# Performance work log

Hardware: AMD Instinct MI355X
Metric: run time of the kernel (lower is better)

## Reference

```python
import jax, jax.numpy as jnp
import numpy as np

MAX_ITER = 3
DAMPING = 1e-3
HUBER_B = 0.02
LAMBDA_ICP, LAMBDA_RGB = 1.0, 1e-6
DIST_THRESH = 0.1


def pixel_grid(H, W):
    j, i = jnp.meshgrid(jnp.arange(H, dtype=jnp.float32), jnp.arange(W, dtype=jnp.float32), indexing='ij')
    return i, j  # i = x (col), j = y (row)


def compute_vertex(depth, K):
    fx, fy, cx, cy = K[0, 0], K[1, 1], K[0, 2], K[1, 2]
    H, W = depth.shape
    i, j = pixel_grid(H, W)
    return jnp.stack([(i - cx) / fx, (j - cy) / fy, jnp.ones_like(i)], -1) * depth[..., None]


def sobel(img, normalize=True):
    # replicate-padded 3x3 Sobel cross-correlation, img [H,W,C]
    p = jnp.pad(img, ((1, 1), (1, 1), (0, 0)), mode='edge')
    dx = (p[:-2, 2:] - p[:-2, :-2]) + 2.0 * (p[1:-1, 2:] - p[1:-1, :-2]) + (p[2:, 2:] - p[2:, :-2])
    dy = (p[2:, :-2] - p[:-2, :-2]) + 2.0 * (p[2:, 1:-1] - p[:-2, 1:-1]) + (p[2:, 2:] - p[:-2, 2:])
    if normalize:
        mag = jnp.sqrt(dx * dx + dy * dy + 1e-8)
        dx, dy = dx / mag, dy / mag
    return dx, dy


def compute_normal(vmap_):
    dx, dy = sobel(vmap_, normalize=False)
    n = jnp.cross(dx, dy)
    n = n / (jnp.linalg.norm(n, axis=-1, keepdims=True) + 1e-8)
    d = vmap_[..., 2]
    invalid = (d <= d.min()) | (d >= d.max())
    return jnp.where(invalid[..., None], 0.0, n)


def warp_jacobian(depth, K):
    fx, fy, cx, cy = K[0, 0], K[1, 1], K[0, 2], K[1, 2]
    H, W = depth.shape
    i, j = pixel_grid(H, W)
    x = (i - cx) / fx * depth
    y = (j - cy) / fy * depth
    invD = 1.0 / depth
    invD2 = invD * invD
    xy = x * y
    O = jnp.zeros_like(depth)
    dx_dp = jnp.stack([-invD2 * xy, 1.0 + x * x * invD2, -y * invD, invD, O, -invD2 * x], -1)
    dy_dp = jnp.stack([-1.0 - invD2 * y * y, xy * invD2, x * invD, O, invD, -invD2 * y], -1)
    return dx_dp * fx, dy_dp * fy


def bilinear(feat, u, v):
    # grid_sample(mode=bilinear, padding=border, align_corners=True) on pixel coords
    H, W, _ = feat.shape
    u = jnp.clip(u, 0.0, W - 1.0)
    v = jnp.clip(v, 0.0, H - 1.0)
    u0 = jnp.floor(u)
    v0 = jnp.floor(v)
    wu = (u - u0)[..., None]
    wv = (v - v0)[..., None]
    u0i = u0.astype(jnp.int32)
    v0i = v0.astype(jnp.int32)
    u1i = jnp.minimum(u0i + 1, W - 1)
    v1i = jnp.minimum(v0i + 1, H - 1)
    f00 = feat[v0i, u0i]
    f01 = feat[v0i, u1i]
    f10 = feat[v1i, u0i]
    f11 = feat[v1i, u1i]
    return (f00 * (1 - wu) + f01 * wu) * (1 - wv) + (f10 * (1 - wu) + f11 * wu) * wv


def project(vt, K, H, W):
    z = vt[..., 2]
    u = vt[..., 0] / z * K[0, 0] + K[0, 2]
    v = vt[..., 1] / z * K[1, 1] + K[1, 2]
    inview = (u > 0) & (u < W - 1) & (v > 0) & (v < H - 1) & (z > 0)
    return u, v, inview


def huber_weight(x, b=HUBER_B):
    rho = jnp.where(x <= b, x * x, 2.0 * b * x - b * b)
    x_safe = jnp.where(x < 1e-8, 1.0, x)
    return jnp.sqrt(rho + 1e-16) / x_safe


def skew(w):
    z = jnp.zeros((), w.dtype)
    return jnp.stack([jnp.stack([z, -w[2], w[1]]), jnp.stack([w[2], z, -w[0]]), jnp.stack([-w[1], w[0], z])])


def exp_so3(w):
    Wh = skew(w)
    th2 = jnp.maximum(jnp.sum(w * w), 1e-30)
    th = jnp.sqrt(th2)
    R = jnp.eye(3, dtype=w.dtype) + Wh * (jnp.sin(th) / th) + (Wh @ Wh) * ((1.0 - jnp.cos(th)) / th2)
    return jnp.where(th <= 1e-10, jnp.eye(3, dtype=w.dtype), R)


def icp_residuals(vertex0, vertex1, normal1, mask0, pose, K):
    H, W, _ = vertex0.shape
    R, t = pose[:3, :3], pose[:3, 3]
    v0t = vertex0 @ R.T + t  # [H,W,3]
    u, v, inview = project(v0t, K, H, W)
    v1w = bilinear(vertex1, u, v)
    n1w = bilinear(normal1, u, v)
    diff = v0t - v1w
    valid = inview & mask0 & (v1w[..., 2] > 0) & (jnp.linalg.norm(diff, axis=-1) < DIST_THRESH)
    res = jnp.where(valid, jnp.sum(n1w * diff, -1), 0.0)  # point-to-plane
    J = jnp.where(valid[..., None], jnp.concatenate([jnp.cross(v0t, n1w), n1w], -1), 0.0)  # [H,W,6]
    w = huber_weight(jnp.abs(res))
    return (w * res).reshape(-1, 1), (w[..., None] * J).reshape(-1, 1, 6)


def rgb_residuals(pose, vertex0, x0, x1, K, mask0):
    H, W, _ = x0.shape
    R, t = pose[:3, :3], pose[:3, 3]
    v0t = vertex0 @ R.T + t
    u, v, inview = project(v0t, K, H, W)
    x1w = bilinear(x1, u, v)
    invalid = (~inview) | (~mask0)
    res = jnp.where(invalid[..., None], 0.0, x1w - x0)
    return res, invalid


def inverse_update_pose(Hm, Rhs, pose):
    xi = (jnp.linalg.inv(Hm) @ Rhs).reshape(-1)
    dR = exp_so3(-xi[:3])
    dt = -dR @ xi[3:]
    R1 = dR @ pose[:3, :3]
    t1 = dR @ pose[:3, 3] + dt
    top = jnp.concatenate([R1, t1[:, None]], 1)
    return jnp.concatenate([top, pose[3:4, :]], 0)


def color_icp(pose10, depth0, depth1, x0, x1, K):
    H, W, C = x0.shape
    vertex0 = compute_vertex(depth0, K)
    normal0 = compute_normal(vertex0)  # computed as in original
    mask0 = depth0 > 0.0
    vertex1 = compute_vertex(depth1, K)
    normal1 = compute_normal(vertex1)
    # pre-computable inverse-compositional RGB jacobian: normalized image grads x warp jacobian
    gx, gy = sobel(x0, normalize=True)  # [H,W,C]
    Jx, Jy = warp_jacobian(depth0, K)  # [H,W,6]
    J_rgb_pre = gx[..., None] * Jx[:, :, None, :] + gy[..., None] * Jy[:, :, None, :]  # [H,W,C,6]
    pose = pose10
    for _ in range(MAX_ITER):
        r_icp, J_icp = icp_residuals(vertex0, vertex1, normal1, mask0, pose, K)
        JtWJ = LAMBDA_ICP * jnp.einsum('nci,ncj->ij', J_icp, J_icp)
        JtR = LAMBDA_ICP * jnp.einsum('nci,nc->i', J_icp, r_icp)
        r_rgb, invalid = rgb_residuals(pose, vertex0, x0, x1, K, mask0)
        J_rgb = jnp.where(invalid[..., None, None], 0.0, J_rgb_pre).reshape(-1, C, 6)
        JtWJ = JtWJ + LAMBDA_RGB * jnp.einsum('nci,ncj->ij', J_rgb, J_rgb)
        JtR = JtR + LAMBDA_RGB * jnp.einsum('nci,nc->i', J_rgb, r_rgb.reshape(-1, C))
        Hm = JtWJ + jnp.eye(6) * (jnp.trace(JtWJ) * DAMPING)  # Levenberg-Marquardt damping
        pose = inverse_update_pose(Hm, JtR.reshape(6, 1), pose)
    return pose


def setup_inputs() -> dict:
    key = jax.random.key(0)
    k = jax.random.split(key, 6)
    H, W = 960, 1280
    depth0 = 0.5 + 2.5 * jax.random.uniform(k[0], (H, W), jnp.float32)
    depth1 = 0.5 + 2.5 * jax.random.uniform(k[1], (H, W), jnp.float32)
    x0 = jax.random.uniform(k[2], (H, W, 3), jnp.float32)
    x1 = jax.random.uniform(k[3], (H, W, 3), jnp.float32)
    K = jnp.array([[1050.0, 0.0, (W - 1) / 2.0], [0.0, 1050.0, (H - 1) / 2.0], [0.0, 0.0, 1.0]], jnp.float32)
    w = 0.01 * jax.random.normal(k[4], (3,), jnp.float32)
    t = 0.01 * jax.random.normal(k[5], (3,), jnp.float32)
    R = exp_so3(w)
    pose10 = jnp.concatenate([jnp.concatenate([R, t[:, None]], 1),
                              jnp.array([[0.0, 0.0, 0.0, 1.0]], jnp.float32)], 0)
    return {'pose10': pose10, 'depth0': depth0, 'depth1': depth1, 'x0': x0, 'x1': x1, 'K': K}


def reference(pose10, depth0, depth1, x0, x1, K):
    return color_icp(pose10, depth0, depth1, x0, x1, K)
```

## Files before the change

kernel.cpp:

```cpp
#include <hip/hip_runtime.h>
#include <math.h>

#define HH 960
#define WW 1280
#define NPIX (HH*WW)
#define BPR (WW/256)
#define NBLK_ROW (NPIX/256)
#define NBLK_MAIN (NPIX/(256*4))
#define TROWS 6
#define TW 258
#define PSTRIDE 28

#define WS_POSE_OFF    0
#define WS_PARTIAL_OFF 128
#define WS_NX_OFF      134528

__device__ __forceinline__ int clampi(int v, int lo, int hi){ return v<lo?lo:(v>hi?hi:v); }

__device__ __forceinline__ float pack2h(float a, float b){
  _Float16 ha = (_Float16)a, hb = (_Float16)b;
  unsigned int u = ((unsigned int)__builtin_bit_cast(unsigned short, hb) << 16)
                 |  (unsigned int)__builtin_bit_cast(unsigned short, ha);
  return __builtin_bit_cast(float, u);
}
__device__ __forceinline__ float2 unpack2h(float p){
  unsigned int u = __builtin_bit_cast(unsigned int, p);
  _Float16 ha = __builtin_bit_cast(_Float16, (unsigned short)(u & 0xffffu));
  _Float16 hb = __builtin_bit_cast(_Float16, (unsigned short)(u >> 16));
  return make_float2((float)ha, (float)hb);
}

__global__ __launch_bounds__(256) void k_pre(const float* __restrict__ depth1,
                                             const float* __restrict__ x1,
                                             const float* __restrict__ Kd,
                                             const float* __restrict__ pose_in,
                                             float* __restrict__ pose,
                                             float* __restrict__ nx1){
  int t = threadIdx.x;
  if (blockIdx.x == 0 && t < 16) pose[t] = pose_in[t];
  int bid = blockIdx.x;
  int py = bid / BPR;
  int px = (bid % BPR)*256 + t;
  float fx = Kd[0], fy = Kd[4], cx = Kd[2], cy = Kd[5];
  float invfx = 1.f/fx, invfy = 1.f/fy;
  float vx[3][3], vy[3][3], vz[3][3];
  #pragma unroll
  for (int dr = 0; dr < 3; dr++){
    int r = clampi(py + dr - 1, 0, HH-1);
    #pragma unroll
    for (int dc = 0; dc < 3; dc++){
      int c = clampi(px + dc - 1, 0, WW-1);
      float d = depth1[r*WW + c];
      vx[dr][dc] = ((float)c - cx)*invfx*d;
      vy[dr][dc] = ((float)r - cy)*invfy*d;
      vz[dr][dc] = d;
    }
  }
  float ax_ = (vx[0][2]-vx[0][0]) + 2.f*(vx[1][2]-vx[1][0]) + (vx[2][2]-vx[2][0]);
  float ay_ = (vy[0][2]-vy[0][0]) + 2.f*(vy[1][2]-vy[1][0]) + (vy[2][2]-vy[2][0]);
  float az_ = (vz[0][2]-vz[0][0]) + 2.f*(vz[1][2]-vz[1][0]) + (vz[2][2]-vz[2][0]);
  float bx_ = (vx[2][0]-vx[0][0]) + 2.f*(vx[2][1]-vx[0][1]) + (vx[2][2]-vx[0][2]);
  float by_ = (vy[2][0]-vy[0][0]) + 2.f*(vy[2][1]-vy[0][1]) + (vy[2][2]-vy[0][2]);
  float bz_ = (vz[2][0]-vz[0][0]) + 2.f*(vz[2][1]-vz[0][1]) + (vz[2][2]-vz[0][2]);
  float nx = ay_*bz_ - az_*by_;
  float ny = az_*bx_ - ax_*bz_;
  float nz = ax_*by_ - ay_*bx_;
  float nrm = sqrtf(nx*nx + ny*ny + nz*nz) + 1e-8f;
  float rn  = __builtin_amdgcn_rcpf(nrm);
  nx *= rn; ny *= rn; nz *= rn;
  float dcen = vz[1][1];
  int idx = py*WW + px;
  const float* q = &x1[idx*3];
  float4 a;
  a.x = dcen;
  a.y = pack2h(nx, ny);
  a.z = pack2h(nz, q[0]);
  a.w = pack2h(q[1], q[2]);
  ((float4*)nx1)[idx] = a;
}

__global__ __launch_bounds__(256) void k_main(const float* __restrict__ depth0,
                                              const float* __restrict__ x0,
                                              const float* __restrict__ nx1,
                                              const float* __restrict__ Kd,
                                              const float* __restrict__ pose,
                                              float* __restrict__ partial){
  int t = threadIdx.x;
  int bid = (blockIdx.x & 7)*(NBLK_MAIN/8) + (blockIdx.x >> 3);
  int pr = bid / BPR;
  int cs = bid % BPR;
  int py0 = pr*4;
  int colbase = cs*256 - 1;
  int px = cs*256 + t;

  __shared__ float tile[TROWS*TW*3];
  for (int s = t; s < TROWS*TW; s += 256){
    int r = s / TW, c = s - r*TW;
    int gr = clampi(py0 - 1 + r, 0, HH-1);
    int gc = clampi(colbase + c, 0, WW-1);
    const float* q = &x0[(gr*WW + gc)*3];
    tile[s*3+0] = q[0]; tile[s*3+1] = q[1]; tile[s*3+2] = q[2];
  }

  int idx0 = py0*WW + px;
  float d0v[4];
  #pragma unroll
  for (int kp = 0; kp < 4; kp++) d0v[kp] = depth0[idx0 + kp*WW];
  __syncthreads();

  float fx = Kd[0], fy = Kd[4], cx = Kd[2], cy = Kd[5];
  float inv_fx = 1.f/fx, inv_fy = 1.f/fy;
  float R00=pose[0], R01=pose[1], R02=pose[2],  tx=pose[3];
  float R10=pose[4], R11=pose[5], R12=pose[6],  ty=pose[7];
  float R20=pose[8], R21=pose[9], R22=pose[10], tz=pose[11];

  float acc[27];
  #pragma unroll
  for (int k = 0; k < 27; k++) acc[k] = 0.f;

  const float4* nx4 = (const float4*)nx1;

  #pragma unroll
  for (int kp = 0; kp < 4; kp++){
    int py = py0 + kp;

    float d0 = d0v[kp];
    bool m0 = d0 > 0.f;
    float v0x = ((float)px - cx)*inv_fx*d0;
    float v0y = ((float)py - cy)*inv_fy*d0;
    float v0z = d0;
    float X = R00*v0x + R01*v0y + R02*v0z + tx;
    float Y = R10*v0x + R11*v0y + R12*v0z + ty;
    float Z = R20*v0x + R21*v0y + R22*v0z + tz;
    float invZ = __builtin_amdgcn_rcpf(Z);
    invZ = invZ*(2.0f - Z*invZ);
    float u = X*invZ*fx + cx;
    float v = Y*invZ*fy + cy;
    bool inview = (u > 0.f) && (u < (float)(WW-1)) && (v > 0.f) && (v < (float)(HH-1)) && (Z > 0.f);

    float uc = fminf(fmaxf(u, 0.f), (float)(WW-1));
    float vc = fminf(fmaxf(v, 0.f), (float)(HH-1));
    float u0f = floorf(uc), v0f = floorf(vc);
    float wu = uc - u0f, wv = vc - v0f;
    int u0i = clampi((int)u0f, 0, WW-1);
    int v0i = clampi((int)v0f, 0, HH-1);
    int u1i = min(u0i + 1, WW-1);
    int v1i = min(v0i + 1, HH-1);
    int i00 = v0i*WW + u0i, i01 = v0i*WW + u1i, i10 = v1i*WW + u0i, i11 = v1i*WW + u1i;
    float w00 = (1.f-wu)*(1.f-wv), w01 = wu*(1.f-wv), w10 = (1.f-wu)*wv, w11 = wu*wv;

    float4 p00 = nx4[i00], p01 = nx4[i01], p10 = nx4[i10], p11v = nx4[i11];

    float2 nab00 = unpack2h(p00.y), nzr00 = unpack2h(p00.z);
    float2 nab01 = unpack2h(p01.y), nzr01 = unpack2h(p01.z);
    float2 nab10 = unpack2h(p10.y), nzr10 = unpack2h(p10.z);
    float2 nab11 = unpack2h(p11v.y), nzr11 = unpack2h(p11v.z);

    float t0 = w00*p00.x, t1 = w01*p01.x, t2 = w10*p10.x, t3 = w11*p11v.x;
    float u0c = ((float)u0i - cx)*inv_fx, u1c = ((float)u1i - cx)*inv_fx;
    float v0c = ((float)v0i - cy)*inv_fy, v1c = ((float)v1i - cy)*inv_fy;
    float s2 = (t0+t1)+(t2+t3);
    float s0 = u0c*(t0+t2) + u1c*(t1+t3);
    float s1 = v0c*(t0+t1) + v1c*(t2+t3);
    float nx = nab00.x*w00 + nab01.x*w01 + nab10.x*w10 + nab11.x*w11;
    float ny = nab00.y*w00 + nab01.y*w01 + nab10.y*w10 + nab11.y*w11;
    float nz = nzr00.x*w00 + nzr01.x*w01 + nzr10.x*w10 + nzr11.x*w11;

    float dfx = X - s0, dfy = Y - s1, dfz = Z - s2;
    bool valid = inview && m0 && (s2 > 0.f) && (dfx*dfx + dfy*dfy + dfz*dfz < 0.01f);
    float res = 0.f;
    float J[6] = {0.f,0.f,0.f,0.f,0.f,0.f};
    if (valid){
      res = nx*dfx + ny*dfy + nz*dfz;
      J[0] = Y*nz - Z*ny;
      J[1] = Z*nx - X*nz;
      J[2] = X*ny - Y*nx;
      J[3] = nx; J[4] = ny; J[5] = nz;
    }
    float axv = fabsf(res);
    float rho = (axv <= 0.02f) ? axv*axv : (0.04f*axv - 0.0004f);
    float xs  = (axv < 1e-8f) ? 1.f : axv;
    float hw  = sqrtf(rho + 1e-16f) * __builtin_amdgcn_rcpf(xs);
    float wr  = hw*res;
    float wJ[6];
    #pragma unroll
    for (int i = 0; i < 6; i++) wJ[i] = hw*J[i];
    {
      int k = 0;
      #pragma unroll
      for (int i = 0; i < 6; i++)
        #pragma unroll
        for (int j = i; j < 6; j++)
          acc[k++] += wJ[i]*wJ[j];
      #pragma unroll
      for (int i = 0; i < 6; i++) acc[21+i] += wJ[i]*wr;
    }

    if (inview && m0){
      float2 gb00 = unpack2h(p00.w), gb01 = unpack2h(p01.w);
      float2 gb10 = unpack2h(p10.w), gb11 = unpack2h(p11v.w);
      float xw[3];
      xw[0] = nzr00.y*w00 + nzr01.y*w01 + nzr10.y*w10 + nzr11.y*w11;
      xw[1] = gb00.x*w00 + gb01.x*w01 + gb10.x*w10 + gb11.x*w11;
      xw[2] = gb00.y*w00 + gb01.y*w01 + gb10.y*w10 + gb11.y*w11;

      float ga = 0.f, gb = 0.f, gc2 = 0.f, rx = 0.f, ry = 0.f;
      #pragma unroll
      for (int ch = 0; ch < 3; ch++){
        float p00l = tile[((kp+0)*TW + (t+0))*3 + ch];
        float p01l = tile[((kp+0)*TW + (t+1))*3 + ch];
        float p02l = tile[((kp+0)*TW + (t+2))*3 + ch];
        float p10l = tile[((kp+1)*TW + (t+0))*3 + ch];
        float p11l = tile[((kp+1)*TW + (t+1))*3 + ch];
        float p12l = tile[((kp+1)*TW + (t+2))*3 + ch];
        float p20l = tile[((kp+2)*TW + (t+0))*3 + ch];
        float p21l = tile[((kp+2)*TW + (t+1))*3 + ch];
        float p22l = tile[((kp+2)*TW + (t+2))*3 + ch];
        float dx = (p02l-p00l) + 2.f*(p12l-p10l) + (p22l-p20l);
        float dy = (p20l-p00l) + 2.f*(p21l-p01l) + (p22l-p02l);
        float rinv = __builtin_amdgcn_rsqf(dx*dx + dy*dy + 1e-8f);
        float gx = dx*rinv, gy = dy*rinv;
        float rr = xw[ch] - p11l;
        ga  += gx*gx; gb += gx*gy; gc2 += gy*gy;
        rx  += gx*rr; ry += gy*rr;
      }
      ga *= 1e-6f; gb *= 1e-6f; gc2 *= 1e-6f; rx *= 1e-6f; ry *= 1e-6f;

      float invD = __builtin_amdgcn_rcpf(d0), invD2 = invD*invD;
      float xy = v0x*v0y;
      float Jx[6] = { fx*(-invD2*xy), fx*(1.f + v0x*v0x*invD2), fx*(-v0y*invD), fx*invD, 0.f, fx*(-invD2*v0x) };
      float Jy[6] = { fy*(-1.f - invD2*v0y*v0y), fy*(xy*invD2), fy*(v0x*invD), 0.f, fy*invD, fy*(-invD2*v0y) };
      float P[6], Q[6];
      #pragma unroll
      for (int i = 0; i < 6; i++){ P[i] = ga*Jx[i] + gb*Jy[i]; Q[i] = gb*Jx[i] + gc2*Jy[i]; }
      int k = 0;
      #pragma unroll
      for (int i = 0; i < 6; i++)
        #pragma unroll
        for (int j = i; j < 6; j++)
          acc[k++] += Jx[j]*P[i] + Jy[j]*Q[i];
      #pragma unroll
      for (int i = 0; i < 6; i++) acc[21+i] += Jx[i]*rx + Jy[i]*ry;
    }
  }

  __shared__ float lds[108];
  int lane = t & 63;
  int wid  = t >> 6;
  #pragma unroll
  for (int k = 0; k < 27; k++){
    float vv = acc[k];
    vv += __shfl_down(vv, 32); vv += __shfl_down(vv, 16); vv += __shfl_down(vv, 8);
    vv += __shfl_down(vv, 4);  vv += __shfl_down(vv, 2);  vv += __shfl_down(vv, 1);
    if (lane == 0) lds[wid*27 + k] = vv;
  }
  __syncthreads();
  if (t < 27)
    partial[bid*PSTRIDE + t] = lds[t] + lds[27+t] + lds[54+t] + lds[81+t];
  else if (t == 27)
    partial[bid*PSTRIDE + 27] = 0.f;
}

__global__ __launch_bounds__(256) void k_solve(const float* __restrict__ partial,
                                               float* __restrict__ pose,
                                               float* __restrict__ outp){
  int t = threadIdx.x;
  double acc[PSTRIDE];
  #pragma unroll
  for (int k = 0; k < PSTRIDE; k++) acc[k] = 0.0;
  const float4* p4 = (const float4*)partial;
  for (int r = t; r < NBLK_MAIN; r += 256){
    #pragma unroll
    for (int q = 0; q < 7; q++){
      float4 vv = p4[r*7 + q];
      acc[q*4+0] += (double)vv.x;
      acc[q*4+1] += (double)vv.y;
      acc[q*4+2] += (double)vv.z;
      acc[q*4+3] += (double)vv.w;
    }
  }
  __shared__ double lds[4*PSTRIDE];
  int lane = t & 63, wid = t >> 6;
  #pragma unroll
  for (int k = 0; k < PSTRIDE; k++){
    double vv = acc[k];
    vv += __shfl_down(vv, 32); vv += __shfl_down(vv, 16); vv += __shfl_down(vv, 8);
    vv += __shfl_down(vv, 4);  vv += __shfl_down(vv, 2);  vv += __shfl_down(vv, 1);
    if (lane == 0) lds[wid*PSTRIDE + k] = vv;
  }
  __syncthreads();
  if (t == 0){
    double s[PSTRIDE];
    #pragma unroll
    for (int k = 0; k < PSTRIDE; k++)
      s[k] = lds[k] + lds[PSTRIDE+k] + lds[2*PSTRIDE+k] + lds[3*PSTRIDE+k];
    double Hm[6][6], b[6];
    {
      int k = 0;
      for (int i = 0; i < 6; i++)
        for (int j = i; j < 6; j++){ Hm[i][j] = s[k]; Hm[j][i] = s[k]; k++; }
      for (int i = 0; i < 6; i++) b[i] = s[21+i];
    }
    double tr = Hm[0][0]+Hm[1][1]+Hm[2][2]+Hm[3][3]+Hm[4][4]+Hm[5][5];
    for (int i = 0; i < 6; i++) Hm[i][i] += tr*0.001;
    double A[6][7];
    for (int i = 0; i < 6; i++){
      for (int j = 0; j < 6; j++) A[i][j] = Hm[i][j];
      A[i][6] = b[i];
    }
    for (int c = 0; c < 6; c++){
      int piv = c; double best = fabs(A[c][c]);
      for (int r = c+1; r < 6; r++){ double a = fabs(A[r][c]); if (a > best){ best = a; piv = r; } }
      if (piv != c)
        for (int j = 0; j < 7; j++){ double tv = A[c][j]; A[c][j] = A[piv][j]; A[piv][j] = tv; }
      double inv = 1.0/A[c][c];
      for (int r = 0; r < 6; r++){
        if (r == c) continue;
        double f = A[r][c]*inv;
        for (int j = c; j < 7; j++) A[r][j] -= f*A[c][j];
      }
    }
    double xi[6];
    for (int i = 0; i < 6; i++) xi[i] = A[i][6]/A[i][i];
    double wx = -xi[0], wy = -xi[1], wz = -xi[2];
    double th2 = wx*wx + wy*wy + wz*wz;
    if (th2 < 1e-30) th2 = 1e-30;
    double th = sqrt(th2);
    double dR[3][3];
    if (th <= 1e-10){
      dR[0][0]=1; dR[0][1]=0; dR[0][2]=0;
      dR[1][0]=0; dR[1][1]=1; dR[1][2]=0;
      dR[2][0]=0; dR[2][1]=0; dR[2][2]=1;
    } else {
      double sa = sin(th)/th;
      double sb = (1.0 - cos(th))/th2;
      double Wm[3][3] = {{0,-wz,wy},{wz,0,-wx},{-wy,wx,0}};
      double W2[3][3];
      for (int i = 0; i < 3; i++)
        for (int j = 0; j < 3; j++)
          W2[i][j] = Wm[i][0]*Wm[0][j] + Wm[i][1]*Wm[1][j] + Wm[i][2]*Wm[2][j];
      for (int i = 0; i < 3; i++)
        for (int j = 0; j < 3; j++)
          dR[i][j] = (i==j ? 1.0 : 0.0) + sa*Wm[i][j] + sb*W2[i][j];
    }
    double dt[3];
    for (int i = 0; i < 3; i++)
      dt[i] = -(dR[i][0]*xi[3] + dR[i][1]*xi[4] + dR[i][2]*xi[5]);
    double Ro[3][3], to[3];
    for (int i = 0; i < 3; i++){
      for (int j = 0; j < 3; j++) Ro[i][j] = (double)pose[i*4+j];
      to[i] = (double)pose[i*4+3];
    }
    double Rn[3][3], tn[3];
    for (int i = 0; i < 3; i++){
      for (int j = 0; j < 3; j++)
        Rn[i][j] = dR[i][0]*Ro[0][j] + dR[i][1]*Ro[1][j] + dR[i][2]*Ro[2][j];
      tn[i] = dR[i][0]*to[0] + dR[i][1]*to[1] + dR[i][2]*to[2] + dt[i];
    }
    float o16[16];
    for (int i = 0; i < 3; i++){
      for (int j = 0; j < 3; j++) o16[i*4+j] = (float)Rn[i][j];
      o16[i*4+3] = (float)tn[i];
    }
    o16[12] = 0.f; o16[13] = 0.f; o16[14] = 0.f; o16[15] = 1.f;
    for (int k = 0; k < 16; k++){ pose[k] = o16[k]; outp[k] = o16[k]; }
  }
}

extern "C" void kernel_launch(void* const* d_in, const int* in_sizes, int n_in,
                              void* d_out, int out_size, void* d_ws, size_t ws_size,
                              hipStream_t stream) {
  const float* pose10 = (const float*)d_in[0];
  const float* depth0 = (const float*)d_in[1];
  const float* depth1 = (const float*)d_in[2];
  const float* x0     = (const float*)d_in[3];
  const float* x1     = (const float*)d_in[4];
  const float* Kd     = (const float*)d_in[5];
  char* ws = (char*)d_ws;
  float* pose    = (float*)(ws + WS_POSE_OFF);
  float* partial = (float*)(ws + WS_PARTIAL_OFF);
  float* nx1     = (float*)(ws + WS_NX_OFF);
  float* outp    = (float*)d_out;

  hipLaunchKernelGGL(k_pre, dim3(NBLK_ROW), dim3(256), 0, stream,
                     depth1, x1, Kd, pose10, pose, nx1);
  for (int it = 0; it < 3; it++){
    hipLaunchKernelGGL(k_main,  dim3(NBLK_MAIN), dim3(256), 0, stream,
                       depth0, x0, nx1, Kd, pose, partial);
    hipLaunchKernelGGL(k_solve, dim3(1),         dim3(256), 0, stream, partial, pose, outp);
  }
}
```

Before: 218.8 us.

## Replace per-iteration solve kernels with atomic sums and redundant in-block pose solve

Each k_main block now atomically adds its 27 reduced sums into a small per-iteration buffer. At the start of each iteration, one wave per block replays the chain of 6x6 solves and pose updates from the original pose, which removes the separate single-block solve launch between iterations. A single final solve kernel writes the output pose. The cost is float atomics, which make summation order nondeterministic, a solve done in float rather than double without pivoting, and redundant solve work in every block.

```diff
diff --git a/kernel.cpp b/kernel.cpp
--- a/kernel.cpp
+++ b/kernel.cpp
@@ -9,11 +9,9 @@
 #define NBLK_MAIN (NPIX/(256*4))
 #define TROWS 6
 #define TW 258
-#define PSTRIDE 28
-
-#define WS_POSE_OFF    0
-#define WS_PARTIAL_OFF 128
-#define WS_NX_OFF      134528
+
+#define WS_S_OFF   0
+#define WS_NX_OFF  512
 
 __device__ __forceinline__ int clampi(int v, int lo, int hi){ return v<lo?lo:(v>hi?hi:v); }
 
@@ -30,14 +28,84 @@
   return make_float2((float)ha, (float)hb);
 }
 
+__device__ __forceinline__ void wave_chain_solve(const float* __restrict__ S, int nsteps,
+                                                 const float* __restrict__ pose_in,
+                                                 float* sp, int lane){
+  if (lane < 12) sp[lane] = pose_in[lane];
+  int r = lane < 6 ? lane : 5;
+  for (int step = 0; step < nsteps; ++step){
+    const float* s = S + step*32;
+    float a[7];
+    #pragma unroll
+    for (int j = 0; j < 6; j++){
+      int i = r < j ? r : j, J = r < j ? j : r;
+      a[j] = s[6*i - (i*(i-1))/2 + (J - i)];
+    }
+    a[6] = s[21 + r];
+    float tr = s[0]+s[6]+s[11]+s[15]+s[18]+s[20];
+    float damp = tr*0.001f;
+    #pragma unroll
+    for (int j = 0; j < 6; j++) a[j] += (r == j) ? damp : 0.f;
+    float mydiag = 1.f;
+    #pragma unroll
+    for (int c = 0; c < 6; c++){
+      float pv[7];
+      #pragma unroll
+      for (int j = 0; j < 7; j++) pv[j] = __shfl(a[j], c);
+      float f = a[c] * (1.0f/pv[c]);
+      bool self = (r == c);
+      if (self) mydiag = a[c];
+      float fr = self ? 0.f : f;
+      #pragma unroll
+      for (int j = 0; j < 7; j++) a[j] -= fr*pv[j];
+    }
+    float xir = a[6] / mydiag;
+    float xi[6];
+    #pragma unroll
+    for (int j = 0; j < 6; j++) xi[j] = __shfl(xir, j);
+    float wx = -xi[0], wy = -xi[1], wz = -xi[2];
+    float th2 = wx*wx + wy*wy + wz*wz; if (th2 < 1e-30f) th2 = 1e-30f;
+    float th = sqrtf(th2);
+    float dR[9];
+    if (th <= 1e-10f){
+      dR[0]=1.f;dR[1]=0.f;dR[2]=0.f; dR[3]=0.f;dR[4]=1.f;dR[5]=0.f; dR[6]=0.f;dR[7]=0.f;dR[8]=1.f;
+    } else {
+      float sa = sinf(th)/th, sb = (1.f - cosf(th))/th2;
+      float cI = 1.f - sb*th2;
+      dR[0]=cI + sb*wx*wx;    dR[1]=sb*wx*wy - sa*wz; dR[2]=sb*wx*wz + sa*wy;
+      dR[3]=sb*wy*wx + sa*wz; dR[4]=cI + sb*wy*wy;    dR[5]=sb*wy*wz - sa*wx;
+      dR[6]=sb*wz*wx - sa*wy; dR[7]=sb*wz*wy + sa*wx; dR[8]=cI + sb*wz*wz;
+    }
+    float dt0 = -(dR[0]*xi[3] + dR[1]*xi[4] + dR[2]*xi[5]);
+    float dt1 = -(dR[3]*xi[3] + dR[4]*xi[4] + dR[5]*xi[5]);
+    float dt2 = -(dR[6]*xi[3] + dR[7]*xi[4] + dR[8]*xi[5]);
+    float Ro[12];
+    #pragma unroll
+    for (int j = 0; j < 12; j++) Ro[j] = sp[j];
+    float Pn[12];
+    #pragma unroll
+    for (int i = 0; i < 3; i++){
+      #pragma unroll
+      for (int j = 0; j < 3; j++)
+        Pn[i*4+j] = dR[i*3+0]*Ro[0*4+j] + dR[i*3+1]*Ro[1*4+j] + dR[i*3+2]*Ro[2*4+j];
+      Pn[i*4+3] = dR[i*3+0]*Ro[3] + dR[i*3+1]*Ro[7] + dR[i*3+2]*Ro[11]
+                + (i==0 ? dt0 : (i==1 ? dt1 : dt2));
+    }
+    if (lane == 0){
+      sp[0]=Pn[0]; sp[1]=Pn[1]; sp[2]=Pn[2];  sp[3]=Pn[3];
+      sp[4]=Pn[4]; sp[5]=Pn[5]; sp[6]=Pn[6];  sp[7]=Pn[7];
+      sp[8]=Pn[8]; sp[9]=Pn[9]; sp[10]=Pn[10]; sp[11]=Pn[11];
+    }
+  }
+}
+
 __global__ __launch_bounds__(256) void k_pre(const float* __restrict__ depth1,
                                              const float* __restrict__ x1,
                                              const float* __restrict__ Kd,
-                                             const float* __restrict__ pose_in,
-                                             float* __restrict__ pose,
+                                             float* __restrict__ S,
                                              float* __restrict__ nx1){
   int t = threadIdx.x;
-  if (blockIdx.x == 0 && t < 16) pose[t] = pose_in[t];
+  if (blockIdx.x == 0 && t < 96) S[t] = 0.f;
   int bid = blockIdx.x;
   int py = bid / BPR;
   int px = (bid % BPR)*256 + t;
@@ -83,8 +151,9 @@
                                               const float* __restrict__ x0,
                                               const float* __restrict__ nx1,
                                               const float* __restrict__ Kd,
-                                              const float* __restrict__ pose,
-                                              float* __restrict__ partial){
+                                              const float* __restrict__ pose10,
+                                              float* __restrict__ S,
+                                              int it){
   int t = threadIdx.x;
   int bid = (blockIdx.x & 7)*(NBLK_MAIN/8) + (blockIdx.x >> 3);
   int pr = bid / BPR;
@@ -94,6 +163,7 @@
   int px = cs*256 + t;
 
   __shared__ float tile[TROWS*TW*3];
+  __shared__ float sp[12];
   for (int s = t; s < TROWS*TW; s += 256){
     int r = s / TW, c = s - r*TW;
     int gr = clampi(py0 - 1 + r, 0, HH-1);
@@ -106,13 +176,15 @@
   float d0v[4];
   #pragma unroll
   for (int kp = 0; kp < 4; kp++) d0v[kp] = depth0[idx0 + kp*WW];
+
+  if (t < 64) wave_chain_solve(S, it, pose10, sp, t);
   __syncthreads();
 
   float fx = Kd[0], fy = Kd[4], cx = Kd[2], cy = Kd[5];
   float inv_fx = 1.f/fx, inv_fy = 1.f/fy;
-  float R00=pose[0], R01=pose[1], R02=pose[2],  tx=pose[3];
-  float R10=pose[4], R11=pose[5], R12=pose[6],  ty=pose[7];
-  float R20=pose[8], R21=pose[9], R22=pose[10], tz=pose[11];
+  float R00=sp[0], R01=sp[1], R02=sp[2],  tx=sp[3];
+  float R10=sp[4], R11=sp[5], R12=sp[6],  ty=sp[7];
+  float R20=sp[8], R21=sp[9], R22=sp[10], tz=sp[11];
 
   float acc[27];
   #pragma unroll
@@ -256,114 +328,19 @@
   }
   __syncthreads();
   if (t < 27)
-    partial[bid*PSTRIDE + t] = lds[t] + lds[27+t] + lds[54+t] + lds[81+t];
-  else if (t == 27)
-    partial[bid*PSTRIDE + 27] = 0.f;
-}
-
-__global__ __launch_bounds__(256) void k_solve(const float* __restrict__ partial,
-                                               float* __restrict__ pose,
-                                               float* __restrict__ outp){
+    atomicAdd(&S[it*32 + t], lds[t] + lds[27+t] + lds[54+t] + lds[81+t]);
+}
+
+__global__ __launch_bounds__(64) void k_solve(const float* __restrict__ S,
+                                              const float* __restrict__ pose10,
+                                              float* __restrict__ outp){
+  __shared__ float sp[12];
   int t = threadIdx.x;
-  double acc[PSTRIDE];
-  #pragma unroll
-  for (int k = 0; k < PSTRIDE; k++) acc[k] = 0.0;
-  const float4* p4 = (const float4*)partial;
-  for (int r = t; r < NBLK_MAIN; r += 256){
-    #pragma unroll
-    for (int q = 0; q < 7; q++){
-      float4 vv = p4[r*7 + q];
-      acc[q*4+0] += (double)vv.x;
-      acc[q*4+1] += (double)vv.y;
-      acc[q*4+2] += (double)vv.z;
-      acc[q*4+3] += (double)vv.w;
-    }
-  }
-  __shared__ double lds[4*PSTRIDE];
-  int lane = t & 63, wid = t >> 6;
-  #pragma unroll
-  for (int k = 0; k < PSTRIDE; k++){
-    double vv = acc[k];
-    vv += __shfl_down(vv, 32); vv += __shfl_down(vv, 16); vv += __shfl_down(vv, 8);
-    vv += __shfl_down(vv, 4);  vv += __shfl_down(vv, 2);  vv += __shfl_down(vv, 1);
-    if (lane == 0) lds[wid*PSTRIDE + k] = vv;
-  }
-  __syncthreads();
+  wave_chain_solve(S, 3, pose10, sp, t);
   if (t == 0){
-    double s[PSTRIDE];
-    #pragma unroll
-    for (int k = 0; k < PSTRIDE; k++)
-      s[k] = lds[k] + lds[PSTRIDE+k] + lds[2*PSTRIDE+k] + lds[3*PSTRIDE+k];
-    double Hm[6][6], b[6];
-    {
-      int k = 0;
-      for (int i = 0; i < 6; i++)
-        for (int j = i; j < 6; j++){ Hm[i][j] = s[k]; Hm[j][i] = s[k]; k++; }
-      for (int i = 0; i < 6; i++) b[i] = s[21+i];
-    }
-    double tr = Hm[0][0]+Hm[1][1]+Hm[2][2]+Hm[3][3]+Hm[4][4]+Hm[5][5];
-    for (int i = 0; i < 6; i++) Hm[i][i] += tr*0.001;
-    double A[6][7];
-    for (int i = 0; i < 6; i++){
-      for (int j = 0; j < 6; j++) A[i][j] = Hm[i][j];
-      A[i][6] = b[i];
-    }
-    for (int c = 0; c < 6; c++){
-      int piv = c; double best = fabs(A[c][c]);
-      for (int r = c+1; r < 6; r++){ double a = fabs(A[r][c]); if (a > best){ best = a; piv = r; } }
-      if (piv != c)
-        for (int j = 0; j < 7; j++){ double tv = A[c][j]; A[c][j] = A[piv][j]; A[piv][j] = tv; }
-      double inv = 1.0/A[c][c];
-      for (int r = 0; r < 6; r++){
-        if (r == c) continue;
-        double f = A[r][c]*inv;
-        for (int j = c; j < 7; j++) A[r][j] -= f*A[c][j];
-      }
-    }
-    double xi[6];
-    for (int i = 0; i < 6; i++) xi[i] = A[i][6]/A[i][i];
-    double wx = -xi[0], wy = -xi[1], wz = -xi[2];
-    double th2 = wx*wx + wy*wy + wz*wz;
-    if (th2 < 1e-30) th2 = 1e-30;
-    double th = sqrt(th2);
-    double dR[3][3];
-    if (th <= 1e-10){
-      dR[0][0]=1; dR[0][1]=0; dR[0][2]=0;
-      dR[1][0]=0; dR[1][1]=1; dR[1][2]=0;
-      dR[2][0]=0; dR[2][1]=0; dR[2][2]=1;
-    } else {
-      double sa = sin(th)/th;
-      double sb = (1.0 - cos(th))/th2;
-      double Wm[3][3] = {{0,-wz,wy},{wz,0,-wx},{-wy,wx,0}};
-      double W2[3][3];
-      for (int i = 0; i < 3; i++)
-        for (int j = 0; j < 3; j++)
-          W2[i][j] = Wm[i][0]*Wm[0][j] + Wm[i][1]*Wm[1][j] + Wm[i][2]*Wm[2][j];
-      for (int i = 0; i < 3; i++)
-        for (int j = 0; j < 3; j++)
-          dR[i][j] = (i==j ? 1.0 : 0.0) + sa*Wm[i][j] + sb*W2[i][j];
-    }
-    double dt[3];
-    for (int i = 0; i < 3; i++)
-      dt[i] = -(dR[i][0]*xi[3] + dR[i][1]*xi[4] + dR[i][2]*xi[5]);
-    double Ro[3][3], to[3];
-    for (int i = 0; i < 3; i++){
-      for (int j = 0; j < 3; j++) Ro[i][j] = (double)pose[i*4+j];
-      to[i] = (double)pose[i*4+3];
-    }
-    double Rn[3][3], tn[3];
-    for (int i = 0; i < 3; i++){
-      for (int j = 0; j < 3; j++)
-        Rn[i][j] = dR[i][0]*Ro[0][j] + dR[i][1]*Ro[1][j] + dR[i][2]*Ro[2][j];
-      tn[i] = dR[i][0]*to[0] + dR[i][1]*to[1] + dR[i][2]*to[2] + dt[i];
-    }
-    float o16[16];
-    for (int i = 0; i < 3; i++){
-      for (int j = 0; j < 3; j++) o16[i*4+j] = (float)Rn[i][j];
-      o16[i*4+3] = (float)tn[i];
-    }
-    o16[12] = 0.f; o16[13] = 0.f; o16[14] = 0.f; o16[15] = 1.f;
-    for (int k = 0; k < 16; k++){ pose[k] = o16[k]; outp[k] = o16[k]; }
+    #pragma unroll
+    for (int k = 0; k < 12; k++) outp[k] = sp[k];
+    outp[12] = 0.f; outp[13] = 0.f; outp[14] = 0.f; outp[15] = 1.f;
   }
 }
 
@@ -377,16 +354,15 @@
   const float* x1     = (const float*)d_in[4];
   const float* Kd     = (const float*)d_in[5];
   char* ws = (char*)d_ws;
-  float* pose    = (float*)(ws + WS_POSE_OFF);
-  float* partial = (float*)(ws + WS_PARTIAL_OFF);
-  float* nx1     = (float*)(ws + WS_NX_OFF);
-  float* outp    = (float*)d_out;
+  float* S    = (float*)(ws + WS_S_OFF);
+  float* nx1  = (float*)(ws + WS_NX_OFF);
+  float* outp = (float*)d_out;
 
   hipLaunchKernelGGL(k_pre, dim3(NBLK_ROW), dim3(256), 0, stream,
-                     depth1, x1, Kd, pose10, pose, nx1);
+                     depth1, x1, Kd, S, nx1);
   for (int it = 0; it < 3; it++){
-    hipLaunchKernelGGL(k_main,  dim3(NBLK_MAIN), dim3(256), 0, stream,
-                       depth0, x0, nx1, Kd, pose, partial);
-    hipLaunchKernelGGL(k_solve, dim3(1),         dim3(256), 0, stream, partial, pose, outp);
-  }
-}
+    hipLaunchKernelGGL(k_main, dim3(NBLK_MAIN), dim3(256), 0, stream,
+                       depth0, x0, nx1, Kd, pose10, S, it);
+  }
+  hipLaunchKernelGGL(k_solve, dim3(1), dim3(64), 0, stream, S, pose10, outp);
+}
```

New measurement: 222.5 us. About the same (+1.7%).

## Precompute normalized Sobel gradients of x0 once in pre-pass, drop LDS tile

Applied to the files above, without the earlier changes.

The normalized Sobel gradients of the source image and the gradient-dot-center terms are now computed once in the pre-pass and packed as fp16 into a 16-byte record per pixel. The main kernel, which runs three times, reads this record instead of staging an x0 tile in shared memory and recomputing the stencil. This removes the shared-memory staging, the barrier and the repeated stencil arithmetic. The cost is an extra buffer write in the pre-pass, and the fp16 packing adds precision loss to the gradients and the C1/C2 terms.

```diff
diff --git a/kernel.cpp b/kernel.cpp
--- a/kernel.cpp
+++ b/kernel.cpp
@@ -7,13 +7,12 @@
 #define BPR (WW/256)
 #define NBLK_ROW (NPIX/256)
 #define NBLK_MAIN (NPIX/(256*4))
-#define TROWS 6
-#define TW 258
 #define PSTRIDE 28
 
 #define WS_POSE_OFF    0
 #define WS_PARTIAL_OFF 128
 #define WS_NX_OFF      134528
+#define WS_REC_OFF     19795328
 
 __device__ __forceinline__ int clampi(int v, int lo, int hi){ return v<lo?lo:(v>hi?hi:v); }
 
@@ -31,56 +30,95 @@
 }
 
 __global__ __launch_bounds__(256) void k_pre(const float* __restrict__ depth1,
+                                             const float* __restrict__ x0,
                                              const float* __restrict__ x1,
                                              const float* __restrict__ Kd,
                                              const float* __restrict__ pose_in,
                                              float* __restrict__ pose,
-                                             float* __restrict__ nx1){
+                                             float* __restrict__ nx1,
+                                             float* __restrict__ rec0){
   int t = threadIdx.x;
   if (blockIdx.x == 0 && t < 16) pose[t] = pose_in[t];
   int bid = blockIdx.x;
   int py = bid / BPR;
   int px = (bid % BPR)*256 + t;
+  int idx = py*WW + px;
   float fx = Kd[0], fy = Kd[4], cx = Kd[2], cy = Kd[5];
   float invfx = 1.f/fx, invfy = 1.f/fy;
-  float vx[3][3], vy[3][3], vz[3][3];
-  #pragma unroll
-  for (int dr = 0; dr < 3; dr++){
-    int r = clampi(py + dr - 1, 0, HH-1);
+
+  {
+    float vx[3][3], vy[3][3], vz[3][3];
     #pragma unroll
-    for (int dc = 0; dc < 3; dc++){
-      int c = clampi(px + dc - 1, 0, WW-1);
-      float d = depth1[r*WW + c];
-      vx[dr][dc] = ((float)c - cx)*invfx*d;
-      vy[dr][dc] = ((float)r - cy)*invfy*d;
-      vz[dr][dc] = d;
-    }
-  }
-  float ax_ = (vx[0][2]-vx[0][0]) + 2.f*(vx[1][2]-vx[1][0]) + (vx[2][2]-vx[2][0]);
-  float ay_ = (vy[0][2]-vy[0][0]) + 2.f*(vy[1][2]-vy[1][0]) + (vy[2][2]-vy[2][0]);
-  float az_ = (vz[0][2]-vz[0][0]) + 2.f*(vz[1][2]-vz[1][0]) + (vz[2][2]-vz[2][0]);
-  float bx_ = (vx[2][0]-vx[0][0]) + 2.f*(vx[2][1]-vx[0][1]) + (vx[2][2]-vx[0][2]);
-  float by_ = (vy[2][0]-vy[0][0]) + 2.f*(vy[2][1]-vy[0][1]) + (vy[2][2]-vy[0][2]);
-  float bz_ = (vz[2][0]-vz[0][0]) + 2.f*(vz[2][1]-vz[0][1]) + (vz[2][2]-vz[0][2]);
-  float nx = ay_*bz_ - az_*by_;
-  float ny = az_*bx_ - ax_*bz_;
-  float nz = ax_*by_ - ay_*bx_;
-  float nrm = sqrtf(nx*nx + ny*ny + nz*nz) + 1e-8f;
-  float rn  = __builtin_amdgcn_rcpf(nrm);
-  nx *= rn; ny *= rn; nz *= rn;
-  float dcen = vz[1][1];
-  int idx = py*WW + px;
-  const float* q = &x1[idx*3];
-  float4 a;
-  a.x = dcen;
-  a.y = pack2h(nx, ny);
-  a.z = pack2h(nz, q[0]);
-  a.w = pack2h(q[1], q[2]);
-  ((float4*)nx1)[idx] = a;
+    for (int dr = 0; dr < 3; dr++){
+      int r = clampi(py + dr - 1, 0, HH-1);
+      #pragma unroll
+      for (int dc = 0; dc < 3; dc++){
+        int c = clampi(px + dc - 1, 0, WW-1);
+        float d = depth1[r*WW + c];
+        vx[dr][dc] = ((float)c - cx)*invfx*d;
+        vy[dr][dc] = ((float)r - cy)*invfy*d;
+        vz[dr][dc] = d;
+      }
+    }
+    float ax_ = (vx[0][2]-vx[0][0]) + 2.f*(vx[1][2]-vx[1][0]) + (vx[2][2]-vx[2][0]);
+    float ay_ = (vy[0][2]-vy[0][0]) + 2.f*(vy[1][2]-vy[1][0]) + (vy[2][2]-vy[2][0]);
+    float az_ = (vz[0][2]-vz[0][0]) + 2.f*(vz[1][2]-vz[1][0]) + (vz[2][2]-vz[2][0]);
+    float bx_ = (vx[2][0]-vx[0][0]) + 2.f*(vx[2][1]-vx[0][1]) + (vx[2][2]-vx[0][2]);
+    float by_ = (vy[2][0]-vy[0][0]) + 2.f*(vy[2][1]-vy[0][1]) + (vy[2][2]-vy[0][2]);
+    float bz_ = (vz[2][0]-vz[0][0]) + 2.f*(vz[2][1]-vz[0][1]) + (vz[2][2]-vz[0][2]);
+    float nx = ay_*bz_ - az_*by_;
+    float ny = az_*bx_ - ax_*bz_;
+    float nz = ax_*by_ - ay_*bx_;
+    float nrm = sqrtf(nx*nx + ny*ny + nz*nz) + 1e-8f;
+    float rn  = __builtin_amdgcn_rcpf(nrm);
+    nx *= rn; ny *= rn; nz *= rn;
+    float dcen = vz[1][1];
+    const float* q = &x1[idx*3];
+    float4 a;
+    a.x = dcen;
+    a.y = pack2h(nx, ny);
+    a.z = pack2h(nz, q[0]);
+    a.w = pack2h(q[1], q[2]);
+    ((float4*)nx1)[idx] = a;
+  }
+
+  {
+    int rm = clampi(py-1, 0, HH-1), rp = clampi(py+1, 0, HH-1);
+    int cm = clampi(px-1, 0, WW-1), cp = clampi(px+1, 0, WW-1);
+    const float* p00 = &x0[(rm*WW+cm)*3];
+    const float* p01 = &x0[(rm*WW+px)*3];
+    const float* p02 = &x0[(rm*WW+cp)*3];
+    const float* p10 = &x0[(py*WW+cm)*3];
+    const float* p11 = &x0[(py*WW+px)*3];
+    const float* p12 = &x0[(py*WW+cp)*3];
+    const float* p20 = &x0[(rp*WW+cm)*3];
+    const float* p21 = &x0[(rp*WW+px)*3];
+    const float* p22 = &x0[(rp*WW+cp)*3];
+    float gx[3], gy[3];
+    float C1 = 0.f, C2 = 0.f;
+    #pragma unroll
+    for (int ch = 0; ch < 3; ch++){
+      float a00 = p00[ch], a01 = p01[ch], a02 = p02[ch];
+      float a10 = p10[ch],                a12 = p12[ch];
+      float a20 = p20[ch], a21 = p21[ch], a22 = p22[ch];
+      float dx = (a02-a00) + 2.f*(a12-a10) + (a22-a20);
+      float dy = (a20-a00) + 2.f*(a21-a01) + (a22-a02);
+      float rinv = __builtin_amdgcn_rsqf(dx*dx + dy*dy + 1e-8f);
+      gx[ch] = dx*rinv; gy[ch] = dy*rinv;
+      float c = p11[ch];
+      C1 += gx[ch]*c; C2 += gy[ch]*c;
+    }
+    float4 r;
+    r.x = pack2h(gx[0], gy[0]);
+    r.y = pack2h(gx[1], gy[1]);
+    r.z = pack2h(gx[2], gy[2]);
+    r.w = pack2h(C1, C2);
+    ((float4*)rec0)[idx] = r;
+  }
 }
 
 __global__ __launch_bounds__(256) void k_main(const float* __restrict__ depth0,
-                                              const float* __restrict__ x0,
+                                              const float* __restrict__ rec0,
                                               const float* __restrict__ nx1,
                                               const float* __restrict__ Kd,
                                               const float* __restrict__ pose,
@@ -90,23 +128,12 @@
   int pr = bid / BPR;
   int cs = bid % BPR;
   int py0 = pr*4;
-  int colbase = cs*256 - 1;
   int px = cs*256 + t;
-
-  __shared__ float tile[TROWS*TW*3];
-  for (int s = t; s < TROWS*TW; s += 256){
-    int r = s / TW, c = s - r*TW;
-    int gr = clampi(py0 - 1 + r, 0, HH-1);
-    int gc = clampi(colbase + c, 0, WW-1);
-    const float* q = &x0[(gr*WW + gc)*3];
-    tile[s*3+0] = q[0]; tile[s*3+1] = q[1]; tile[s*3+2] = q[2];
-  }
 
   int idx0 = py0*WW + px;
   float d0v[4];
   #pragma unroll
   for (int kp = 0; kp < 4; kp++) d0v[kp] = depth0[idx0 + kp*WW];
-  __syncthreads();
 
   float fx = Kd[0], fy = Kd[4], cx = Kd[2], cy = Kd[5];
   float inv_fx = 1.f/fx, inv_fy = 1.f/fy;
@@ -119,12 +146,14 @@
   for (int k = 0; k < 27; k++) acc[k] = 0.f;
 
   const float4* nx4 = (const float4*)nx1;
+  const float4* rc4 = (const float4*)rec0;
 
   #pragma unroll
   for (int kp = 0; kp < 4; kp++){
     int py = py0 + kp;
 
     float d0 = d0v[kp];
+    float4 rv = rc4[idx0 + kp*WW];
     bool m0 = d0 > 0.f;
     float v0x = ((float)px - cx)*inv_fx*d0;
     float v0y = ((float)py - cy)*inv_fy*d0;
@@ -199,32 +228,17 @@
     if (inview && m0){
       float2 gb00 = unpack2h(p00.w), gb01 = unpack2h(p01.w);
       float2 gb10 = unpack2h(p10.w), gb11 = unpack2h(p11v.w);
-      float xw[3];
-      xw[0] = nzr00.y*w00 + nzr01.y*w01 + nzr10.y*w10 + nzr11.y*w11;
-      xw[1] = gb00.x*w00 + gb01.x*w01 + gb10.x*w10 + gb11.x*w11;
-      xw[2] = gb00.y*w00 + gb01.y*w01 + gb10.y*w10 + gb11.y*w11;
-
-      float ga = 0.f, gb = 0.f, gc2 = 0.f, rx = 0.f, ry = 0.f;
-      #pragma unroll
-      for (int ch = 0; ch < 3; ch++){
-        float p00l = tile[((kp+0)*TW + (t+0))*3 + ch];
-        float p01l = tile[((kp+0)*TW + (t+1))*3 + ch];
-        float p02l = tile[((kp+0)*TW + (t+2))*3 + ch];
-        float p10l = tile[((kp+1)*TW + (t+0))*3 + ch];
-        float p11l = tile[((kp+1)*TW + (t+1))*3 + ch];
-        float p12l = tile[((kp+1)*TW + (t+2))*3 + ch];
-        float p20l = tile[((kp+2)*TW + (t+0))*3 + ch];
-        float p21l = tile[((kp+2)*TW + (t+1))*3 + ch];
-        float p22l = tile[((kp+2)*TW + (t+2))*3 + ch];
-        float dx = (p02l-p00l) + 2.f*(p12l-p10l) + (p22l-p20l);
-        float dy = (p20l-p00l) + 2.f*(p21l-p01l) + (p22l-p02l);
-        float rinv = __builtin_amdgcn_rsqf(dx*dx + dy*dy + 1e-8f);
-        float gx = dx*rinv, gy = dy*rinv;
-        float rr = xw[ch] - p11l;
-        ga  += gx*gx; gb += gx*gy; gc2 += gy*gy;
-        rx  += gx*rr; ry += gy*rr;
-      }
-      ga *= 1e-6f; gb *= 1e-6f; gc2 *= 1e-6f; rx *= 1e-6f; ry *= 1e-6f;
+      float xw0 = nzr00.y*w00 + nzr01.y*w01 + nzr10.y*w10 + nzr11.y*w11;
+      float xw1 = gb00.x*w00 + gb01.x*w01 + gb10.x*w10 + gb11.x*w11;
+      float xw2 = gb00.y*w00 + gb01.y*w01 + gb10.y*w10 + gb11.y*w11;
+
+      float2 g0 = unpack2h(rv.x), g1 = unpack2h(rv.y), g2 = unpack2h(rv.z), cc = unpack2h(rv.w);
+      float ga  = g0.x*g0.x + g1.x*g1.x + g2.x*g2.x;
+      float gbv = g0.x*g0.y + g1.x*g1.y + g2.x*g2.y;
+      float gc2 = g0.y*g0.y + g1.y*g1.y + g2.y*g2.y;
+      float rx  = g0.x*xw0 + g1.x*xw1 + g2.x*xw2 - cc.x;
+      float ry  = g0.y*xw0 + g1.y*xw1 + g2.y*xw2 - cc.y;
+      ga *= 1e-6f; gbv *= 1e-6f; gc2 *= 1e-6f; rx *= 1e-6f; ry *= 1e-6f;
 
       float invD = __builtin_amdgcn_rcpf(d0), invD2 = invD*invD;
       float xy = v0x*v0y;
@@ -232,7 +246,7 @@
       float Jy[6] = { fy*(-1.f - invD2*v0y*v0y), fy*(xy*invD2), fy*(v0x*invD), 0.f, fy*invD, fy*(-invD2*v0y) };
       float P[6], Q[6];
       #pragma unroll
-      for (int i = 0; i < 6; i++){ P[i] = ga*Jx[i] + gb*Jy[i]; Q[i] = gb*Jx[i] + gc2*Jy[i]; }
+      for (int i = 0; i < 6; i++){ P[i] = ga*Jx[i] + gbv*Jy[i]; Q[i] = gbv*Jx[i] + gc2*Jy[i]; }
       int k = 0;
       #pragma unroll
       for (int i = 0; i < 6; i++)
@@ -380,13 +394,14 @@
   float* pose    = (float*)(ws + WS_POSE_OFF);
   float* partial = (float*)(ws + WS_PARTIAL_OFF);
   float* nx1     = (float*)(ws + WS_NX_OFF);
+  float* rec0    = (float*)(ws + WS_REC_OFF);
   float* outp    = (float*)d_out;
 
   hipLaunchKernelGGL(k_pre, dim3(NBLK_ROW), dim3(256), 0, stream,
-                     depth1, x1, Kd, pose10, pose, nx1);
+                     depth1, x0, x1, Kd, pose10, pose, nx1, rec0);
   for (int it = 0; it < 3; it++){
     hipLaunchKernelGGL(k_main,  dim3(NBLK_MAIN), dim3(256), 0, stream,
-                       depth0, x0, nx1, Kd, pose, partial);
+                       depth0, rec0, nx1, Kd, pose, partial);
     hipLaunchKernelGGL(k_solve, dim3(1),         dim3(256), 0, stream, partial, pose, outp);
   }
 }
```

Measured after the change: 215.3 us, median of 2. About the same (-1.6%).
